# Kernel tuning notes

Hardware: AMD Instinct MI355X
Metric: run time of the kernel (lower is better)

## Reference

```python
import jax, jax.numpy as jnp
import numpy as np

EPS = 1e-12  # matches torch F.normalize default eps
SCALE = 64.0  # fixed softmax temperature from the source

def _l2_normalize(x, axis):
    n = jnp.linalg.norm(x, ord=2, axis=axis, keepdims=True)
    return x / jnp.maximum(n, EPS)

def setup_inputs() -> dict:
    key = jax.random.key(0)
    k1, k2, k3 = jax.random.split(key, 3)
    B, L, S, D = 8, 2048, 2048, 128
    return {
        "query": jax.random.normal(k1, (B, L, D), dtype=jnp.float32),
        "key": jax.random.normal(k2, (B, S, D), dtype=jnp.float32),
        "value": jax.random.normal(k3, (B, S, D), dtype=jnp.float32),
    }

def reference(query, key, value):
    # rank-3 query path with norm=True, return_value=True, return_score=False
    q = _l2_normalize(query, axis=2)   # [B, L, D]
    k = _l2_normalize(key, axis=2)     # [B, S, D]
    score = jnp.einsum('nlk,nsk->nls', q, k)            # [B, L, S]
    score = jax.nn.softmax(score * SCALE, axis=2)
    # original does broadcast-multiply-then-sum; equivalent contraction:
    out = jnp.einsum('nls,nsd->nld', score, value)      # [B, L, D]
    return out
```

## Files before the change

kernel.cpp:

```cpp
#include <hip/hip_runtime.h>
#include <stdint.h>

#define Bb 8
#define Ll 2048
#define Ss 2048
#define Dd 128
#define NSB 4
#define SCHUNK 512
#define NROWS 16384
#define SCALE_LOG2E 92.33248261689366f

typedef __attribute__((ext_vector_type(8))) short bf16x8;
typedef __attribute__((ext_vector_type(16))) float f32x16;

__device__ __forceinline__ unsigned f2bf_pack(float a, float b) {
  unsigned ua = __float_as_uint(a); ua += 0x7fffu + ((ua >> 16) & 1u);
  unsigned ub = __float_as_uint(b); ub += 0x7fffu + ((ub >> 16) & 1u);
  return (ua >> 16) | (ub & 0xffff0000u);
}

__device__ __forceinline__ unsigned pkbf(float a, float b) {
#if __has_builtin(__builtin_amdgcn_cvt_pk_bf16_f32)
  auto r = __builtin_amdgcn_cvt_pk_bf16_f32(a, b);
  return __builtin_bit_cast(unsigned, r);
#else
  return f2bf_pack(a, b);
#endif
}

__device__ __forceinline__ void gl_lds16(const void* g, void* l) {
  __builtin_amdgcn_global_load_lds(
      (const __attribute__((address_space(1))) unsigned*)g,
      (__attribute__((address_space(3))) unsigned*)l, 16, 0, 0);
}


extern "C" __global__ __launch_bounds__(256)
void prep_kern(const float* __restrict__ K, const float* __restrict__ V,
               unsigned short* __restrict__ Kf, unsigned short* __restrict__ Vf) {
  __shared__ float Tf[32 * 130];
  __shared__ float Ps[32 * 8];
  __shared__ float Nr[32];
  __shared__ unsigned short Tb[32 * 128];
  const int t = threadIdx.x;
  const int bid = blockIdx.x;
  if (bid < 512) {
    const int kb = bid;
    const int b = kb & 7, sw = kb >> 3;
    const int sl = t >> 3, d0 = (t & 7) * 16;
    const float* src = K + ((size_t)(b * Ss + sw * 32 + sl)) * Dd + d0;
    float ss = 0.f;
#pragma unroll
    for (int i = 0; i < 4; ++i) {
      float4 v = *(const float4*)(src + i * 4);
      Tf[sl * 130 + d0 + i * 4 + 0] = v.x;
      Tf[sl * 130 + d0 + i * 4 + 1] = v.y;
      Tf[sl * 130 + d0 + i * 4 + 2] = v.z;
      Tf[sl * 130 + d0 + i * 4 + 3] = v.w;
      ss += v.x * v.x + v.y * v.y + v.z * v.z + v.w * v.w;
    }
    Ps[sl * 8 + (t & 7)] = ss;
    __syncthreads();
    if (t < 32) {
      float s = 0.f;
#pragma unroll
      for (int j = 0; j < 8; ++j) s += Ps[t * 8 + j];
      Nr[t] = 1.0f / fmaxf(sqrtf(s), 1e-12f);
    }
    __syncthreads();
    unsigned short* Ko = Kf + ((size_t)(b * 64 + sw)) * 4096;
#pragma unroll
    for (int p = 0; p < 2; ++p) {
      const int run = p * 256 + t;
      const int lane = run & 63, s = lane & 31, h = lane >> 5;
      const int d = (run >> 6) * 16 + h * 8;
      const float n = Nr[s];
      const float* row = &Tf[s * 130 + d];
      uint4 w;
      w.x = pkbf(row[0] * n, row[1] * n);
      w.y = pkbf(row[2] * n, row[3] * n);
      w.z = pkbf(row[4] * n, row[5] * n);
      w.w = pkbf(row[6] * n, row[7] * n);
      *(uint4*)(Ko + run * 8) = w;
    }
  } else {
    const int vb = bid - 512;
    const int b = vb & 7, sw = vb >> 3;
    const int sl = t >> 3, d0 = (t & 7) * 16;
    const float* src = V + ((size_t)(b * Ss + sw * 32 + sl)) * Dd + d0;
#pragma unroll
    for (int i = 0; i < 4; ++i) {
      float4 v = *(const float4*)(src + i * 4);
      *(unsigned*)&Tb[sl * 128 + d0 + i * 4]     = pkbf(v.x, v.y);
      *(unsigned*)&Tb[sl * 128 + d0 + i * 4 + 2] = pkbf(v.z, v.w);
    }
    __syncthreads();
    unsigned short* Vo = Vf + ((size_t)(b * 64 + sw)) * 4096;
#pragma unroll
    for (int p = 0; p < 2; ++p) {
      const int run = p * 256 + t;
      const int vslot = run >> 6, lane = run & 63;
      const int dloc = lane & 31, h = lane >> 5;
      const int dblk = vslot >> 1, t2 = vslot & 1;
      const int d = dblk * 32 + dloc;
      unsigned short w[8];
#pragma unroll
      for (int j = 0; j < 8; ++j) {
        const int sloc = t2 * 16 + 4 * h + (j & 3) + 8 * (j >> 2);
        w[j] = Tb[sloc * 128 + d];
      }
      *(uint4*)(Vo + run * 8) = *(uint4*)w;
    }
  }
}

extern "C" __global__ __launch_bounds__(256, 2)
void attn_kern(const float* __restrict__ Q,
               const unsigned short* __restrict__ Kf,
               const unsigned short* __restrict__ Vf,
               unsigned short* __restrict__ Op,
               float* __restrict__ Lp) {
  __shared__ unsigned short Kl[4][8 * 512];
  __shared__ unsigned short Vl[4][8 * 512];
  const int tid = threadIdx.x, wv = tid >> 6, lane = tid & 63;
  const int lm = lane & 31, h = lane >> 5;
  const int gid = blockIdx.x;
  const int qt = gid >> 5, b = (gid >> 2) & 7, sb = gid & 3;
  const int sblk0 = sb * (SCHUNK / 32);
  const int qrow = qt * 128 + wv * 32 + lm;

  const float* Qr = Q + ((size_t)(b * Ll + qrow)) * Dd;
  float qv[8][8];
  float ss = 0.f;
#pragma unroll
  for (int kt = 0; kt < 8; ++kt) {
    const float* cp = Qr + kt * 16 + h * 8;
    float4 u0 = *(const float4*)cp;
    float4 u1 = *(const float4*)(cp + 4);
    qv[kt][0] = u0.x; qv[kt][1] = u0.y; qv[kt][2] = u0.z; qv[kt][3] = u0.w;
    qv[kt][4] = u1.x; qv[kt][5] = u1.y; qv[kt][6] = u1.z; qv[kt][7] = u1.w;
    ss += u0.x * u0.x + u0.y * u0.y + u0.z * u0.z + u0.w * u0.w +
          u1.x * u1.x + u1.y * u1.y + u1.z * u1.z + u1.w * u1.w;
  }
  ss += __shfl_xor(ss, 32, 64);
  const float qinv = 1.0f / fmaxf(sqrtf(ss), 1e-12f);
  bf16x8 qf[8];
#pragma unroll
  for (int kt = 0; kt < 8; ++kt) {
    uint4 w;
    w.x = pkbf(qv[kt][0] * qinv, qv[kt][1] * qinv);
    w.y = pkbf(qv[kt][2] * qinv, qv[kt][3] * qinv);
    w.z = pkbf(qv[kt][4] * qinv, qv[kt][5] * qinv);
    w.w = pkbf(qv[kt][6] * qinv, qv[kt][7] * qinv);
    qf[kt] = __builtin_bit_cast(bf16x8, w);
  }

  const unsigned short* Kc = Kf + ((size_t)(b * 64 + sblk0)) * 4096;
  const unsigned short* Vc = Vf + ((size_t)(b * 64 + sblk0)) * 4096;

  f32x16 o[4];
#pragma unroll
  for (int i = 0; i < 4; ++i)
#pragma unroll
    for (int r = 0; r < 16; ++r) o[i][r] = 0.f;

  auto stage = [&](int t, int r) {
    const unsigned short* kb = Kc + (size_t)t * 4096;
    const unsigned short* vb = Vc + (size_t)t * 4096;
#pragma unroll
    for (int i = 0; i < 2; ++i) {
      const int sl = wv * 2 + i;
      gl_lds16(kb + sl * 512 + lane * 8, &Kl[r][sl * 512]);
      gl_lds16(vb + sl * 512 + lane * 8, &Vl[r][sl * 512]);
    }
  };
  stage(0, 0);
  stage(1, 1);

  float lrun = 0.f;

#pragma unroll 1
  for (int it = 0; it < 16; ++it) {
    if (it < 15)
      asm volatile("s_waitcnt vmcnt(4)\n\ts_barrier" ::: "memory");
    else
      asm volatile("s_waitcnt vmcnt(0)\n\ts_barrier" ::: "memory");
    const int r = it & 3;
    if (it + 2 < 16) stage(it + 2, (it + 2) & 3);

    f32x16 acc;
#pragma unroll
    for (int rr = 0; rr < 16; ++rr) acc[rr] = 0.f;
#pragma unroll
    for (int kt = 0; kt < 8; ++kt) {
      bf16x8 kf = *(const bf16x8*)&Kl[r][kt * 512 + lane * 8];
      acc = __builtin_amdgcn_mfma_f32_32x32x16_bf16(kf, qf[kt], acc, 0, 0, 0);
    }
#pragma unroll
    for (int t2 = 0; t2 < 2; ++t2) {
      float p[8];
#pragma unroll
      for (int j = 0; j < 8; ++j)
        p[j] = __builtin_amdgcn_exp2f(
            __builtin_fmaf(acc[t2 * 8 + j], SCALE_LOG2E, -SCALE_LOG2E));
      lrun += ((p[0] + p[1]) + (p[2] + p[3])) + ((p[4] + p[5]) + (p[6] + p[7]));
      uint4 fr;
      fr.x = pkbf(p[0], p[1]);
      fr.y = pkbf(p[2], p[3]);
      fr.z = pkbf(p[4], p[5]);
      fr.w = pkbf(p[6], p[7]);
      bf16x8 pf = __builtin_bit_cast(bf16x8, fr);
#pragma unroll
      for (int dblk = 0; dblk < 4; ++dblk) {
        bf16x8 vf = *(const bf16x8*)&Vl[r][(dblk * 2 + t2) * 512 + lane * 8];
        o[dblk] = __builtin_amdgcn_mfma_f32_32x32x16_bf16(vf, pf, o[dblk], 0, 0, 0);
      }
    }
  }

  const float lt = lrun + __shfl_xor(lrun, 32, 64);
  unsigned short* Ob = Op + ((size_t)sb * NROWS + b * Ll + qrow) * Dd;
#pragma unroll
  for (int dblk = 0; dblk < 4; ++dblk)
#pragma unroll
    for (int g = 0; g < 4; ++g) {
      uint2 w;
      w.x = pkbf(o[dblk][g * 4 + 0], o[dblk][g * 4 + 1]);
      w.y = pkbf(o[dblk][g * 4 + 2], o[dblk][g * 4 + 3]);
      *(uint2*)(Ob + dblk * 32 + g * 8 + h * 4) = w;
    }
  if (h == 0) Lp[sb * NROWS + b * Ll + qrow] = lt;
}

extern "C" __global__ __launch_bounds__(256)
void comb_kern(const unsigned short* __restrict__ Op,
               const float* __restrict__ Lp, float* __restrict__ Out) {
  const int idx = blockIdx.x * 256 + threadIdx.x;
  const int row = idx >> 4;
  const int dof = (idx & 15) * 8;
  float den = 0.f;
#pragma unroll
  for (int s = 0; s < NSB; ++s) den += Lp[s * NROWS + row];
  float a[8] = {0.f, 0.f, 0.f, 0.f, 0.f, 0.f, 0.f, 0.f};
#pragma unroll
  for (int s = 0; s < NSB; ++s) {
    uint4 v = *(const uint4*)(Op + ((size_t)s * NROWS + row) * Dd + dof);
    a[0] += __uint_as_float(v.x << 16);
    a[1] += __uint_as_float(v.x & 0xffff0000u);
    a[2] += __uint_as_float(v.y << 16);
    a[3] += __uint_as_float(v.y & 0xffff0000u);
    a[4] += __uint_as_float(v.z << 16);
    a[5] += __uint_as_float(v.z & 0xffff0000u);
    a[6] += __uint_as_float(v.w << 16);
    a[7] += __uint_as_float(v.w & 0xffff0000u);
  }
  const float inv = 1.f / den;
  float4 r0; r0.x = a[0] * inv; r0.y = a[1] * inv; r0.z = a[2] * inv; r0.w = a[3] * inv;
  float4 r1; r1.x = a[4] * inv; r1.y = a[5] * inv; r1.z = a[6] * inv; r1.w = a[7] * inv;
  float* op = Out + (size_t)row * Dd + dof;
  *(float4*)op = r0;
  *(float4*)(op + 4) = r1;
}

extern "C" void kernel_launch(void* const* d_in, const int* in_sizes, int n_in,
                              void* d_out, int out_size, void* d_ws, size_t ws_size,
                              hipStream_t stream) {
  const float* Q = (const float*)d_in[0];
  const float* K = (const float*)d_in[1];
  const float* V = (const float*)d_in[2];
  float* Out = (float*)d_out;
  unsigned short* Kf = (unsigned short*)d_ws;
  unsigned short* Vf = Kf + (size_t)NROWS * Dd;
  unsigned short* Op = Vf + (size_t)Bb * Dd * Ss;
  float* Lp = (float*)(Op + (size_t)NSB * NROWS * Dd);
  hipLaunchKernelGGL(prep_kern, dim3(1024), dim3(256), 0, stream, K, V, Kf, Vf);
  hipLaunchKernelGGL(attn_kern, dim3(512), dim3(256), 0, stream, Q, Kf, Vf, Op, Lp);
  hipLaunchKernelGGL(comb_kern, dim3(1024), dim3(256), 0, stream, Op, Lp, Out);
}
```

Before: 107.5 us.

## Software-pipeline QK MFMA of the next tile with softmax and PV of the current

Restructures the attention partial-sum loop into a two-stage ping-pong pipeline. Tile t+1's QK^T MFMAs are issued before tile t's exp2, bf16 pack and PV MFMAs, using two alternating accumulators. The goal is to hide exp/VALU latency behind independent matrix-core work rather than serializing QK and softmax within each tile. The cost is an extra 16-float accumulator in registers, which could reduce occupancy or cause spills, and prologue and epilogue code for the 4-slot LDS ring.

```diff
diff --git a/kernel.cpp b/kernel.cpp
--- a/kernel.cpp
+++ b/kernel.cpp
@@ -174,35 +174,27 @@
       gl_lds16(vb + sl * 512 + lane * 8, &Vl[r][sl * 512]);
     }
   };
-  stage(0, 0);
-  stage(1, 1);
 
   float lrun = 0.f;
-
-#pragma unroll 1
-  for (int it = 0; it < 16; ++it) {
-    if (it < 15)
-      asm volatile("s_waitcnt vmcnt(4)\n\ts_barrier" ::: "memory");
-    else
-      asm volatile("s_waitcnt vmcnt(0)\n\ts_barrier" ::: "memory");
-    const int r = it & 3;
-    if (it + 2 < 16) stage(it + 2, (it + 2) & 3);
-
-    f32x16 acc;
-#pragma unroll
-    for (int rr = 0; rr < 16; ++rr) acc[rr] = 0.f;
+  f32x16 accA, accB;
+
+  auto qk = [&](f32x16& a, int slot) {
+#pragma unroll
+    for (int rr = 0; rr < 16; ++rr) a[rr] = 0.f;
 #pragma unroll
     for (int kt = 0; kt < 8; ++kt) {
-      bf16x8 kf = *(const bf16x8*)&Kl[r][kt * 512 + lane * 8];
-      acc = __builtin_amdgcn_mfma_f32_32x32x16_bf16(kf, qf[kt], acc, 0, 0, 0);
-    }
+      bf16x8 kf = *(const bf16x8*)&Kl[slot][kt * 512 + lane * 8];
+      a = __builtin_amdgcn_mfma_f32_32x32x16_bf16(kf, qf[kt], a, 0, 0, 0);
+    }
+  };
+  auto smpv = [&](const f32x16& a, int slot) {
 #pragma unroll
     for (int t2 = 0; t2 < 2; ++t2) {
       float p[8];
 #pragma unroll
       for (int j = 0; j < 8; ++j)
         p[j] = __builtin_amdgcn_exp2f(
-            __builtin_fmaf(acc[t2 * 8 + j], SCALE_LOG2E, -SCALE_LOG2E));
+            __builtin_fmaf(a[t2 * 8 + j], SCALE_LOG2E, -SCALE_LOG2E));
       lrun += ((p[0] + p[1]) + (p[2] + p[3])) + ((p[4] + p[5]) + (p[6] + p[7]));
       uint4 fr;
       fr.x = pkbf(p[0], p[1]);
@@ -212,11 +204,37 @@
       bf16x8 pf = __builtin_bit_cast(bf16x8, fr);
 #pragma unroll
       for (int dblk = 0; dblk < 4; ++dblk) {
-        bf16x8 vf = *(const bf16x8*)&Vl[r][(dblk * 2 + t2) * 512 + lane * 8];
+        bf16x8 vf = *(const bf16x8*)&Vl[slot][(dblk * 2 + t2) * 512 + lane * 8];
         o[dblk] = __builtin_amdgcn_mfma_f32_32x32x16_bf16(vf, pf, o[dblk], 0, 0, 0);
       }
     }
-  }
+  };
+
+  stage(0, 0);
+  stage(1, 1);
+
+  asm volatile("s_waitcnt vmcnt(4)\n\ts_barrier" ::: "memory");
+  stage(2, 2);
+  qk(accA, 0);
+
+#pragma unroll 1
+  for (int i2 = 0; i2 < 7; ++i2) {
+    const int itO = 2 * i2 + 1;
+    asm volatile("s_waitcnt vmcnt(4)\n\ts_barrier" ::: "memory");
+    stage(itO + 2, (itO + 2) & 3);
+    qk(accB, itO & 3);
+    smpv(accA, (itO - 1) & 3);
+    const int itE = itO + 1;
+    asm volatile("s_waitcnt vmcnt(4)\n\ts_barrier" ::: "memory");
+    if (itE + 2 <= 15) stage(itE + 2, (itE + 2) & 3);
+    qk(accA, itE & 3);
+    smpv(accB, (itE - 1) & 3);
+  }
+
+  asm volatile("s_waitcnt vmcnt(0)\n\ts_barrier" ::: "memory");
+  qk(accB, 15 & 3);
+  smpv(accA, 14 & 3);
+  smpv(accB, 15 & 3);
 
   const float lt = lrun + __shfl_xor(lrun, 32, 64);
   unsigned short* Ob = Op + ((size_t)sb * NROWS + b * Ll + qrow) * Dd;
```

After: 106.4 us (median of 2 runs). No clear change (-1.1%).
